# Kernel tuning notes

Hardware: AMD Instinct MI355X
Metric: run time of the kernel (lower is better)

Reference implementation:

```python
import jax, jax.numpy as jnp
import numpy as np

C_IN = 64
GDIM = C_IN // 2      # 32, GHPA dim_in
CD = GDIM // 4        # 8, c_dim_in
GRID = C_IN // 2      # 32, learned param grid (x=y)
EXPR = 2
B, W, H, D = 2, 64, 64, 64


def _gelu(x):
    return jax.nn.gelu(x, approximate=False)


def _interp_last(p, out_len):
    # 1D linear interpolation along last axis, align_corners=True
    L = p.shape[-1]
    pos = jnp.linspace(0.0, L - 1.0, out_len)
    i0 = jnp.clip(jnp.floor(pos).astype(jnp.int32), 0, L - 1)
    i1 = jnp.clip(i0 + 1, 0, L - 1)
    w = (pos - i0).astype(p.dtype)
    return p[..., i0] * (1.0 - w) + p[..., i1] * w


def _interp2(p, h, w):
    # bilinear align_corners=True over last two axes (separable)
    p = _interp_last(p, w)
    p = jnp.swapaxes(_interp_last(jnp.swapaxes(p, -2, -1), h), -2, -1)
    return p


def _conv2d(x, w, b, groups=1, pad=0):
    y = jax.lax.conv_general_dilated(x, w, (1, 1), [(pad, pad), (pad, pad)],
                                     feature_group_count=groups,
                                     dimension_numbers=('NCHW', 'OIHW', 'NCHW'))
    return y + b[None, :, None, None]


def _conv1d(x, w, b, groups=1, pad=0):
    y = jax.lax.conv_general_dilated(x, w, (1,), [(pad, pad)],
                                     feature_group_count=groups,
                                     dimension_numbers=('NCH', 'OIH', 'NCH'))
    return y + b[None, :, None]


def _ln_cf(x, g, b, eps=1e-6):
    # channels_first LayerNorm over channel axis 1 of NCHW
    u = x.mean(1, keepdims=True)
    s = ((x - u) ** 2).mean(1, keepdims=True)
    xh = (x - u) / jnp.sqrt(s + eps)
    return g[None, :, None, None] * xh + b[None, :, None, None]


def _inorm3d(x, eps=1e-5):
    # InstanceNorm3d, affine=False: normalize over spatial dims per (B, C)
    u = x.mean((2, 3, 4), keepdims=True)
    v = ((x - u) ** 2).mean((2, 3, 4), keepdims=True)
    return (x - u) / jnp.sqrt(v + eps)


def setup_inputs() -> dict:
    key = jax.random.key(0)
    ks = iter(jax.random.split(key, 40))
    f = lambda shape: 0.05 * jax.random.normal(next(ks), shape, dtype=jnp.float32)
    z = lambda shape: jnp.zeros(shape, jnp.float32)
    o = lambda shape: jnp.ones(shape, jnp.float32)
    inp = {
        'x': jax.random.normal(next(ks), (B, C_IN, W, H, D), dtype=jnp.float32),
        # GHPA layer norms
        'n1_g': o((GDIM,)), 'n1_b': z((GDIM,)),
        'n2_g': o((GDIM,)), 'n2_b': z((GDIM,)),
        # learned Hadamard params (torch inits to ones)
        'p_xy': o((1, CD, GRID, GRID)),
        'p_zx': o((1, 1, CD, GRID)),
        'p_zy': o((1, 1, CD, GRID)),
        # conv_xy: depthwise 3x3 + 1x1
        'xy_dw_w': f((CD, 1, 3, 3)), 'xy_dw_b': z((CD,)),
        'xy_pw_w': f((CD, CD, 1, 1)), 'xy_pw_b': z((CD,)),
        # conv_zx / conv_zy: depthwise 1d k=3 + 1x1 1d
        'zx_dw_w': f((CD, 1, 3)), 'zx_dw_b': z((CD,)),
        'zx_pw_w': f((CD, CD, 1)), 'zx_pw_b': z((CD,)),
        'zy_dw_w': f((CD, 1, 3)), 'zy_dw_b': z((CD,)),
        'zy_pw_w': f((CD, CD, 1)), 'zy_pw_b': z((CD,)),
        # dw branch: 1x1 + depthwise 3x3
        'dw_pw_w': f((CD, CD, 1, 1)), 'dw_pw_b': z((CD,)),
        'dw_dw_w': f((CD, 1, 3, 3)), 'dw_dw_b': z((CD,)),
        # ldw: depthwise 3x3 + 1x1 on full GDIM
        'ldw_dw_w': f((GDIM, 1, 3, 3)), 'ldw_dw_b': z((GDIM,)),
        'ldw_pw_w': f((GDIM, GDIM, 1, 1)), 'ldw_pw_b': z((GDIM,)),
        # MlpChannel 1x1x1 convs as dense over channel
        'fc1_w': f((C_IN * EXPR, C_IN)), 'fc1_b': z((C_IN * EXPR,)),
        'fc2_w': f((C_IN, C_IN * EXPR)), 'fc2_b': z((C_IN,)),
    }
    return inp


def reference(x, n1_g, n1_b, n2_g, n2_b, p_xy, p_zx, p_zy,
              xy_dw_w, xy_dw_b, xy_pw_w, xy_pw_b,
              zx_dw_w, zx_dw_b, zx_pw_w, zx_pw_b,
              zy_dw_w, zy_dw_b, zy_pw_w, zy_pw_b,
              dw_pw_w, dw_pw_b, dw_dw_w, dw_dw_b,
              ldw_dw_w, ldw_dw_b, ldw_pw_w, ldw_pw_b,
              fc1_w, fc1_b, fc2_w, fc2_b):
    cd = CD

    def ghpa(z):  # z: (N, GDIM, A, Bd)
        N, C, A, Bd = z.shape
        z = _ln_cf(z, n1_g, n1_b)
        x1, x2, x3, x4 = jnp.split(z, 4, axis=1)
        # xy branch: interpolate learned 2D grid, conv, Hadamard
        k = _interp2(p_xy, A, Bd)                       # (1, cd, A, Bd)
        k = _conv2d(k, xy_dw_w, xy_dw_b, groups=cd, pad=1)
        k = _conv2d(_gelu(k), xy_pw_w, xy_pw_b)
        x1 = x1 * k
        # zx branch: permute (N,cd,A,Bd)->(N,Bd,cd,A)
        x2p = jnp.transpose(x2, (0, 3, 1, 2))
        kz = _interp2(p_zx, cd, A)[0]                   # (1, cd, A)
        kz = _conv1d(kz, zx_dw_w, zx_dw_b, groups=cd, pad=1)
        kz = _conv1d(_gelu(kz), zx_pw_w, zx_pw_b)
        x2 = jnp.transpose(x2p * kz[None], (0, 2, 3, 1))
        # zy branch: permute (N,cd,A,Bd)->(N,A,cd,Bd)
        x3p = jnp.transpose(x3, (0, 2, 1, 3))
        ky = _interp2(p_zy, cd, Bd)[0]                  # (1, cd, Bd)
        ky = _conv1d(ky, zy_dw_w, zy_dw_b, groups=cd, pad=1)
        ky = _conv1d(_gelu(ky), zy_pw_w, zy_pw_b)
        x3 = jnp.transpose(x3p * ky[None], (0, 2, 1, 3))
        # dw branch
        x4 = _conv2d(x4, dw_pw_w, dw_pw_b)
        x4 = _conv2d(_gelu(x4), dw_dw_w, dw_dw_b, groups=cd, pad=1)
        z = jnp.concatenate([x1, x2, x3, x4], axis=1)
        z = _ln_cf(z, n2_g, n2_b)
        z = _conv2d(z, ldw_dw_w, ldw_dw_b, groups=GDIM, pad=1)
        z = _conv2d(_gelu(z), ldw_pw_w, ldw_pw_b)
        return z

    xh, xres = jnp.split(x, 2, axis=1)                  # each (B, GDIM, W, H, D)
    xh = _inorm3d(xh)
    Bb, C, Ww, Hh, Dd = xh.shape
    # direction 0: 'b c w h d -> (h b) c w d'
    xr = jnp.transpose(xh, (3, 0, 1, 2, 4)).reshape(Hh * Bb, C, Ww, Dd)
    y1 = ghpa(xr).reshape(Hh, Bb, C, Ww, Dd).transpose(1, 2, 3, 0, 4)
    y2 = ghpa(xr[::-1]).reshape(Hh, Bb, C, Ww, Dd).transpose(1, 2, 3, 0, 4)[::-1]
    whd = y1 + y2
    z = jnp.concatenate([whd, xres], axis=1)            # (B, C_IN, W, H, D)
    z = _inorm3d(z)
    # MlpChannel: 1x1x1 convs = channel-wise dense
    h = jnp.einsum('bcwhd,oc->bowhd', z, fc1_w) + fc1_b[None, :, None, None, None]
    h = _gelu(h)
    out = jnp.einsum('bcwhd,oc->bowhd', h, fc2_w) + fc2_b[None, :, None, None, None]
    return out
```

## Files before the change

### kernel.cpp

```cpp
#include <hip/hip_runtime.h>
#include <hip/hip_bf16.h>

typedef __hip_bfloat16 bf16;
typedef __attribute__((ext_vector_type(8))) short short8;
typedef __attribute__((ext_vector_type(4))) float f32x4;

__device__ __forceinline__ float b2f(bf16 v){ return __bfloat162float(v); }
__device__ __forceinline__ bf16  f2b(float v){ return __float2bfloat16(v); }
__device__ __forceinline__ unsigned short f2bu(float f){
  return __builtin_bit_cast(unsigned short, __float2bfloat16(f));
}
__device__ __forceinline__ float u2f(unsigned short u){
  return __uint_as_float(((unsigned int)u) << 16);
}
__device__ __forceinline__ float geluf(float x){ return 0.5f*x*(1.0f+erff(x*0.70710678118654752440f)); }

template<bool F32> __device__ __forceinline__ float ldin(const void* p, size_t i){
  if (F32) return ((const float*)p)[i];
  return b2f(((const bf16*)p)[i]);
}
__device__ __forceinline__ float ldf(const void* p, size_t i, bool f32){
  return f32 ? ((const float*)p)[i] : b2f(((const bf16*)p)[i]);
}

#define SS    4096
#define SSS   262144

__global__ void k_probe(const unsigned short* __restrict__ xr, int* __restrict__ flag){
  float m = 0.f;
  for (int i = threadIdx.x; i < 512; i += 64){
    unsigned int u = ((unsigned int)xr[i]) << 16;
    float v = fabsf(__uint_as_float(u));
    if (!(v < 3.0e38f)) v = 3.0e38f;
    m = fmaxf(m, v);
  }
  #pragma unroll
  for (int off = 32; off > 0; off >>= 1) m = fmaxf(m, __shfl_down(m, off));
  if (threadIdx.x == 0) flag[0] = (m > 1000.0f) ? 1 : 0;
}

__device__ __forceinline__ void blk_reduce2(float& s, float& s2){
  __shared__ float sa[4], sb[4];
  #pragma unroll
  for (int off = 32; off > 0; off >>= 1){ s += __shfl_down(s, off); s2 += __shfl_down(s2, off); }
  int wid = threadIdx.x >> 6;
  if ((threadIdx.x & 63) == 0){ sa[wid] = s; sb[wid] = s2; }
  __syncthreads();
  if (threadIdx.x == 0){ s = sa[0]+sa[1]+sa[2]+sa[3]; s2 = sb[0]+sb[1]+sb[2]+sb[3]; }
}

__global__ __launch_bounds__(256) void k_cstats(const int* __restrict__ flag,
    const void* __restrict__ x, float* __restrict__ part){
  const bool f32 = (flag[0] != 0);
  int bc = blockIdx.x >> 3, sp = blockIdx.x & 7;
  size_t base = (size_t)bc*SSS + (size_t)sp*32768;
  float s = 0.f, s2 = 0.f;
  if (f32){
    const float4* p = (const float4*)((const float*)x + base);
    for (int i = threadIdx.x; i < 8192; i += 256){
      float4 v = p[i];
      s += v.x+v.y+v.z+v.w; s2 += v.x*v.x+v.y*v.y+v.z*v.z+v.w*v.w;
    }
  } else {
    const ushort4* p = (const ushort4*)((const unsigned short*)x + base);
    for (int i = threadIdx.x; i < 8192; i += 256){
      ushort4 v = p[i];
      float a=u2f(v.x),b_=u2f(v.y),c=u2f(v.z),d=u2f(v.w);
      s += a+b_+c+d; s2 += a*a+b_*b_+c*c+d*d;
    }
  }
  blk_reduce2(s, s2);
  if (threadIdx.x == 0){ part[blockIdx.x*2] = s; part[blockIdx.x*2+1] = s2; }
}

__global__ void k_sfinal(const float* __restrict__ part,
    float* __restrict__ meanH, float* __restrict__ rstdH,
    float* __restrict__ mean2, float* __restrict__ rstd2){
  int t = threadIdx.x; if (t >= 128) return;
  float s = 0.f, s2 = 0.f;
  #pragma unroll
  for (int i = 0; i < 8; i++){ s += part[(t*8+i)*2]; s2 += part[(t*8+i)*2+1]; }
  float m = s * (1.f/262144.f);
  float var = s2 * (1.f/262144.f) - m*m;
  int b = t >> 6, c = t & 63;
  if (c < 32){ meanH[b*32+c] = m; rstdH[b*32+c] = rsqrtf(var + 1e-5f); }
  else       { mean2[t] = m;      rstd2[t] = rsqrtf(var + 1e-5f); }
}

__global__ __launch_bounds__(256) void k_mult1(const int* __restrict__ flag,
    const void* __restrict__ p_xy, const void* __restrict__ p_zx, const void* __restrict__ p_zy,
    const void* __restrict__ xy_dw_w, const void* __restrict__ xy_dw_b,
    const void* __restrict__ zx_dw_w, const void* __restrict__ zx_dw_b,
    const void* __restrict__ zy_dw_w, const void* __restrict__ zy_dw_b,
    float* __restrict__ t_xy, float* __restrict__ t_zx, float* __restrict__ t_zy){
  const bool f32 = (flag[0] != 0);
  const float SC = 31.f/63.f;
  int id = blockIdx.x*256 + threadIdx.x;
  if (id < 32768){
    int c = id >> 12, rem = id & 4095, uu = rem >> 6, vv = rem & 63;
    float acc = ldf(xy_dw_b, c, f32);
    for (int du = 0; du < 3; du++){
      int ui = uu + du - 1; if (ui < 0 || ui >= 64) continue;
      float pu = ui*SC; int i0 = (int)pu; float wu = pu - (float)i0; int i1 = min(i0+1, 31);
      for (int dv = 0; dv < 3; dv++){
        int vi = vv + dv - 1; if (vi < 0 || vi >= 64) continue;
        float pv = vi*SC; int j0 = (int)pv; float wv = pv - (float)j0; int j1 = min(j0+1, 31);
        float s = ldf(p_xy, c*1024+i0*32+j0, f32)*(1.f-wu)*(1.f-wv) + ldf(p_xy, c*1024+i0*32+j1, f32)*(1.f-wu)*wv
                + ldf(p_xy, c*1024+i1*32+j0, f32)*wu*(1.f-wv)       + ldf(p_xy, c*1024+i1*32+j1, f32)*wu*wv;
        acc += ldf(xy_dw_w, c*9 + du*3 + dv, f32) * s;
      }
    }
    t_xy[id] = geluf(acc);
  } else if (id < 33280){
    int k = id - 32768; int c = k >> 6, a = k & 63;
    float acc = ldf(zx_dw_b, c, f32);
    for (int da = 0; da < 3; da++){
      int ai = a + da - 1; if (ai < 0 || ai >= 64) continue;
      float pa = ai*SC; int i0 = (int)pa; float wa = pa - (float)i0; int i1 = min(i0+1, 31);
      float s = ldf(p_zx, c*32+i0, f32)*(1.f-wa) + ldf(p_zx, c*32+i1, f32)*wa;
      acc += ldf(zx_dw_w, c*3+da, f32) * s;
    }
    t_zx[k] = geluf(acc);
  } else if (id < 33792){
    int k = id - 33280; int c = k >> 6, a = k & 63;
    float acc = ldf(zy_dw_b, c, f32);
    for (int da = 0; da < 3; da++){
      int ai = a + da - 1; if (ai < 0 || ai >= 64) continue;
      float pa = ai*SC; int i0 = (int)pa; float wa = pa - (float)i0; int i1 = min(i0+1, 31);
      float s = ldf(p_zy, c*32+i0, f32)*(1.f-wa) + ldf(p_zy, c*32+i1, f32)*wa;
      acc += ldf(zy_dw_w, c*3+da, f32) * s;
    }
    t_zy[k] = geluf(acc);
  }
}

__global__ __launch_bounds__(256) void k_mult2(const int* __restrict__ flag,
    const float* __restrict__ t_xy, const float* __restrict__ t_zx, const float* __restrict__ t_zy,
    const void* __restrict__ xy_pw_w, const void* __restrict__ xy_pw_b,
    const void* __restrict__ zx_pw_w, const void* __restrict__ zx_pw_b,
    const void* __restrict__ zy_pw_w, const void* __restrict__ zy_pw_b,
    float* __restrict__ kxy, float* __restrict__ kz, float* __restrict__ ky){
  const bool f32 = (flag[0] != 0);
  int id = blockIdx.x*256 + threadIdx.x;
  if (id < 32768){
    int oc = id >> 12, pix = id & 4095;
    float acc = ldf(xy_pw_b, oc, f32);
    #pragma unroll
    for (int ic = 0; ic < 8; ic++) acc += ldf(xy_pw_w, oc*8+ic, f32) * t_xy[ic*4096 + pix];
    kxy[id] = acc;
  } else if (id < 33280){
    int k = id - 32768; int oc = k >> 6, a = k & 63;
    float acc = ldf(zx_pw_b, oc, f32);
    #pragma unroll
    for (int ic = 0; ic < 8; ic++) acc += ldf(zx_pw_w, oc*8+ic, f32) * t_zx[ic*64 + a];
    kz[k] = acc;
  } else if (id < 33792){
    int k = id - 33280; int oc = k >> 6, a = k & 63;
    float acc = ldf(zy_pw_b, oc, f32);
    #pragma unroll
    for (int ic = 0; ic < 8; ic++) acc += ldf(zy_pw_w, oc*8+ic, f32) * t_zy[ic*64 + a];
    ky[k] = acc;
  }
}

#define TB 4
#define W_M    0
#define W_R    32
#define W_G1   64
#define W_B1   96
#define W_G2   128
#define W_B2   160
#define W_LDWB 192
#define W_LPWB 224
#define W_PW   256
#define W_PWB  320
#define W_DW   328
#define W_DWB  400
#define W_LDW  408
#define W_TOT  696

template<bool F32>
__global__ __launch_bounds__(256) void k_g(const int* __restrict__ flag,
    const void* __restrict__ x,
    const void* n1g_, const void* n1b_, const void* n2g_, const void* n2b_,
    const void* dwpw_w, const void* dwpw_b, const void* dwdw_w, const void* dwdw_b,
    const void* ldw_dw_w, const void* ldw_dw_b, const void* ldw_pw_w, const void* ldw_pw_b,
    const float* __restrict__ meanH, const float* __restrict__ rstdH,
    const float* __restrict__ kxy, const float* __restrict__ kz, const float* __restrict__ ky,
    bf16* __restrict__ g){
  if (flag[0] != (F32 ? 1 : 0)) return;
  __shared__ unsigned short xs[32*6*64];
  __shared__ unsigned short t4g[8*8*64];
  __shared__ float muinv[2*6*64];
  __shared__ float sw[W_TOT];
  int n  = blockIdx.x >> 4;
  int a0 = (blockIdx.x & 15) * TB;
  int b = n & 1, h = n >> 1;
  int t = threadIdx.x;
  if (t < 32){
    sw[W_M+t]=meanH[b*32+t]; sw[W_R+t]=rstdH[b*32+t];
    sw[W_G1+t]=ldin<F32>(n1g_, t); sw[W_B1+t]=ldin<F32>(n1b_, t);
    sw[W_G2+t]=ldin<F32>(n2g_, t); sw[W_B2+t]=ldin<F32>(n2b_, t);
    sw[W_LDWB+t]=ldin<F32>(ldw_dw_b, t); sw[W_LPWB+t]=ldin<F32>(ldw_pw_b, t);
  }
  if (t >= 64 && t < 128) sw[W_PW+t-64]=ldin<F32>(dwpw_w, t-64);
  if (t >= 128 && t < 200) sw[W_DW+t-128]=ldin<F32>(dwdw_w, t-128);
  if (t >= 200 && t < 208) sw[W_PWB+t-200]=ldin<F32>(dwpw_b, t-200);
  if (t >= 208 && t < 216) sw[W_DWB+t-208]=ldin<F32>(dwdw_b, t-208);
  for (int i = t; i < 288; i += 256)  sw[W_LDW+i] = ldin<F32>(ldw_dw_w, i);
  __syncthreads();
  const float* s_g1 = sw+W_G1; const float* s_b1 = sw+W_B1;
  const float* s_g2 = sw+W_G2; const float* s_b2 = sw+W_B2;
  const int arow0 = a0 - 2;
  const size_t xbase = (size_t)b*64*SSS + (size_t)h*64;

  for (int i = t; i < 3072; i += 256){
    int c = i / 96, rem = i - c*96, row = rem >> 4, q = rem & 15;
    int a = a0 - 1 + row;
    unsigned short o0=0,o1=0,o2=0,o3=0;
    if (a >= 0 && a < 64){
      float m = sw[W_M+c], r = sw[W_R+c];
      size_t base = xbase + (size_t)c*SSS + (size_t)a*SS + q*4;
      if (F32){
        float4 v = *(const float4*)((const float*)x + base);
        o0=f2bu((v.x-m)*r); o1=f2bu((v.y-m)*r); o2=f2bu((v.z-m)*r); o3=f2bu((v.w-m)*r);
      } else {
        ushort4 v = *(const ushort4*)((const unsigned short*)x + base);
        o0=f2bu((u2f(v.x)-m)*r); o1=f2bu((u2f(v.y)-m)*r); o2=f2bu((u2f(v.z)-m)*r); o3=f2bu((u2f(v.w)-m)*r);
      }
    }
    ushort4 o4; o4.x=o0; o4.y=o1; o4.z=o2; o4.w=o3;
    *(ushort4*)&xs[(c*6+row)*64 + q*4] = o4;
  }
  __syncthreads();

  for (int p = t; p < 8*64; p += 256){
    int row = p >> 6, d = p & 63;
    int a = arow0 + row;
    if (a < 0 || a >= 64){
      #pragma unroll
      for (int ic = 0; ic < 8; ic++) t4g[(ic*8+row)*64+d] = 0;
      continue;
    }
    float sum = 0.f, sq = 0.f; float z24[8];
    if (row >= 1 && row <= 6){
      int r6 = row - 1;
      #pragma unroll
      for (int c = 0; c < 32; c++){
        float v = u2f(xs[(c*6+r6)*64+d]); sum += v; sq += v*v;
        if (c >= 24) z24[c-24] = v;
      }
    } else {
      size_t xi = xbase + (size_t)a*SS + d;
      #pragma unroll
      for (int c = 0; c < 32; c++){
        float v = (ldin<F32>(x, xi + (size_t)c*SSS) - sw[W_M+c]) * sw[W_R+c];
        sum += v; sq += v*v;
        if (c >= 24) z24[c-24] = v;
      }
    }
    float mu = sum * (1.f/32.f);
    float inv = rsqrtf(sq*(1.f/32.f) - mu*mu + 1e-6f);
    if (row >= 1 && row <= 6){
      muinv[(row-1)*64+d] = mu; muinv[384 + (row-1)*64+d] = inv;
    }
    float zl[8];
    #pragma unroll
    for (int j = 0; j < 8; j++) zl[j] = (z24[j]-mu)*inv*s_g1[24+j] + s_b1[24+j];
    #pragma unroll
    for (int ic = 0; ic < 8; ic++){
      float acc = sw[W_PWB+ic];
      #pragma unroll
      for (int j = 0; j < 8; j++) acc += sw[W_PW+ic*8+j]*zl[j];
      t4g[(ic*8+row)*64+d] = f2bu(geluf(acc));
    }
  }
  __syncthreads();

  for (int p = t; p < 6*64; p += 256){
    int r2 = p >> 6, d = p & 63;
    int a = a0 - 1 + r2;
    if (a < 0 || a >= 64) continue;
    float mu = muinv[r2*64+d], inv = muinv[384 + r2*64+d];
    float s2 = 0.f, q2 = 0.f;
    #pragma unroll
    for (int c = 0; c < 8; c++){
      int idx = (c*6+r2)*64+d;
      float u = ((u2f(xs[idx])-mu)*inv*s_g1[c] + s_b1[c]) * kxy[(c*64 + a)*64 + d];
      xs[idx] = f2bu(u); s2 += u; q2 += u*u;
    }
    #pragma unroll
    for (int c = 8; c < 16; c++){
      int idx = (c*6+r2)*64+d;
      float u = ((u2f(xs[idx])-mu)*inv*s_g1[c] + s_b1[c]) * kz[(c-8)*64 + a];
      xs[idx] = f2bu(u); s2 += u; q2 += u*u;
    }
    #pragma unroll
    for (int c = 16; c < 24; c++){
      int idx = (c*6+r2)*64+d;
      float u = ((u2f(xs[idx])-mu)*inv*s_g1[c] + s_b1[c]) * ky[(c-16)*64 + d];
      xs[idx] = f2bu(u); s2 += u; q2 += u*u;
    }
    #pragma unroll
    for (int oc = 0; oc < 8; oc++){
      float acc = sw[W_DWB+oc];
      #pragma unroll
      for (int du = 0; du < 3; du++){
        #pragma unroll
        for (int dv = 0; dv < 3; dv++){
          int v2 = d + dv - 1;
          if (v2 >= 0 && v2 < 64) acc += sw[W_DW+oc*9+du*3+dv]*u2f(t4g[(oc*8+r2+du)*64+v2]);
        }
      }
      xs[((24+oc)*6+r2)*64+d] = f2bu(acc); s2 += acc; q2 += acc*acc;
    }
    float mu2 = s2 * (1.f/32.f);
    float inv2 = rsqrtf(q2*(1.f/32.f) - mu2*mu2 + 1e-6f);
    #pragma unroll
    for (int c = 0; c < 32; c++){
      int idx = (c*6+r2)*64+d;
      float uu = u2f(xs[idx]);
      xs[idx] = f2bu((uu-mu2)*inv2*s_g2[c] + s_b2[c]);
    }
  }
  __syncthreads();

  unsigned short* lpwB = t4g;
  unsigned short* gdXS = xs;
  for (int i = t; i < 1024; i += 256){
    int o = i >> 5, ic = i & 31;
    lpwB[o*40 + ic] = f2bu(ldin<F32>(ldw_pw_w, o*32+ic));
  }
  float gd[32];
  {
    int r = t >> 6, d = t & 63;
    #pragma unroll
    for (int oc = 0; oc < 32; oc++){
      float acc = sw[W_LDWB+oc];
      #pragma unroll
      for (int du = 0; du < 3; du++){
        #pragma unroll
        for (int dv = 0; dv < 3; dv++){
          int v2 = d + dv - 1;
          if (v2 >= 0 && v2 < 64) acc += sw[W_LDW+oc*9+du*3+dv]*u2f(xs[(oc*6+r+du)*64+v2]);
        }
      }
      gd[oc] = geluf(acc);
    }
  }
  __syncthreads();

  #pragma unroll
  for (int q = 0; q < 4; q++){
    unsigned short tmp8[8];
    #pragma unroll
    for (int j = 0; j < 8; j++) tmp8[j] = f2bu(gd[q*8+j]);
    *(short8*)&gdXS[t*40 + q*8] = *(const short8*)tmp8;
  }
  __syncthreads();

  {
    int wv = t >> 6, l = t & 63;
    int lr = l & 15, lg = l >> 4;
    #pragma unroll
    for (int mi = 0; mi < 4; mi++){
      int px0 = wv*64 + mi*16;
      short8 af = *(const short8*)&gdXS[(px0+lr)*40 + lg*8];
      #pragma unroll
      for (int ot = 0; ot < 2; ot++){
        short8 bf = *(const short8*)&lpwB[(ot*16+lr)*40 + lg*8];
        f32x4 c4 = {0.f,0.f,0.f,0.f};
        c4 = __builtin_amdgcn_mfma_f32_16x16x32_bf16(af, bf, c4, 0, 0, 0);
        int oc = ot*16 + lr;
        float bo = sw[W_LPWB+oc];
        #pragma unroll
        for (int r4 = 0; r4 < 4; r4++){
          int px = px0 + lg*4 + r4;
          int aa = a0 + (px >> 6), dd = px & 63;
          g[(size_t)n*131072 + (size_t)oc*4096 + aa*64 + dd] = f2b(c4[r4] + bo);
        }
      }
    }
  }
}

__global__ __launch_bounds__(256) void k_gstats(const bf16* __restrict__ g,
                                                float* __restrict__ partg){
  int pair = blockIdx.x >> 3, sp = blockIdx.x & 7;
  int b = pair >> 5, c = pair & 31;
  float s = 0.f, s2 = 0.f;
  for (int i = threadIdx.x; i < 32768; i += 256){
    int ii = sp*32768 + i;
    int d = ii & 63, w = (ii >> 6) & 63, h = ii >> 12;
    int n1 = h*2 + b, n2 = (63-h)*2 + b;
    float v = b2f(g[((size_t)n1*32 + c)*4096 + w*64 + d]) + b2f(g[((size_t)n2*32 + c)*4096 + w*64 + d]);
    s += v; s2 += v*v;
  }
  blk_reduce2(s, s2);
  if (threadIdx.x == 0){ partg[blockIdx.x*2] = s; partg[blockIdx.x*2+1] = s2; }
}

__global__ void k_gfinal(const float* __restrict__ partg,
                         float* __restrict__ mean2, float* __restrict__ rstd2){
  int t = threadIdx.x; if (t >= 64) return;
  float s = 0.f, s2 = 0.f;
  #pragma unroll
  for (int i = 0; i < 8; i++){ s += partg[(t*8+i)*2]; s2 += partg[(t*8+i)*2+1]; }
  float m = s * (1.f/262144.f);
  float var = s2 * (1.f/262144.f) - m*m;
  int b = t >> 5, c = t & 31;
  mean2[b*64+c] = m; rstd2[b*64+c] = rsqrtf(var + 1e-5f);
}

__global__ __launch_bounds__(256) void k_mlp(const int* __restrict__ flag,
    const void* __restrict__ x, const bf16* __restrict__ g,
    const float* __restrict__ mean2, const float* __restrict__ rstd2,
    const void* __restrict__ fc1w, const void* __restrict__ fc1b,
    const void* __restrict__ fc2w, const void* __restrict__ fc2b,
    void* __restrict__ out){
  const bool f32 = (flag[0] != 0);
  __shared__ unsigned short zs[128*72];
  __shared__ unsigned short w1s[128*72];
  __shared__ unsigned short w2s[64*136];
  __shared__ unsigned short hb[4*16*136];
  __shared__ float b1s[128], b2s[64];
  int blk = blockIdx.x;
  int b = blk >> 11, w = (blk >> 5) & 63, hblk = blk & 31;
  int h0 = hblk*2;
  int t = threadIdx.x;
  const float* m2 = mean2 + b*64;
  const float* r2 = rstd2 + b*64;

  if (f32){
    const float* W1 = (const float*)fc1w;
    const float* W2 = (const float*)fc2w;
    for (int i = t; i < 8192; i += 256){ int j = i >> 6, c = i & 63; w1s[j*72+c] = f2bu(W1[i] * r2[c]); }
    for (int i = t; i < 8192; i += 256){ int o = i >> 7, j = i & 127; w2s[o*136+j] = f2bu(W2[i]); }
    if (t < 128){
      float s = 0.f;
      for (int c = 0; c < 64; c++) s += W1[t*64+c] * m2[c] * r2[c];
      b1s[t] = ((const float*)fc1b)[t] - s;
    }
    if (t < 64) b2s[t] = ((const float*)fc2b)[t];
  } else {
    const bf16* W1 = (const bf16*)fc1w;
    const bf16* W2 = (const bf16*)fc2w;
    for (int i = t; i < 8192; i += 256){ int j = i >> 6, c = i & 63; w1s[j*72+c] = f2bu(b2f(W1[i]) * r2[c]); }
    for (int i = t; i < 8192; i += 256){ int o = i >> 7, j = i & 127; w2s[o*136+j] = f2bu(b2f(W2[i])); }
    if (t < 128){
      float s = 0.f;
      for (int c = 0; c < 64; c++) s += b2f(W1[t*64+c]) * m2[c] * r2[c];
      b1s[t] = b2f(((const bf16*)fc1b)[t]) - s;
    }
    if (t < 64) b2s[t] = b2f(((const bf16*)fc2b)[t]);
  }

  {
    int px = t & 127, half = t >> 7;
    int hh = px >> 6, d = px & 63;
    int h = h0 + hh;
    unsigned short tmp[32];
    if (half == 0){
      int n1 = h*2 + b, n2 = (63-h)*2 + b;
      const bf16* g1 = g + ((size_t)n1*32)*4096 + w*64 + d;
      const bf16* g2 = g + ((size_t)n2*32)*4096 + w*64 + d;
      #pragma unroll
      for (int c = 0; c < 32; c++) tmp[c] = f2bu(b2f(g1[(size_t)c*4096]) + b2f(g2[(size_t)c*4096]));
    } else {
      size_t xi = ((size_t)(b*64+32))*SSS + (size_t)w*4096 + (size_t)h*64 + d;
      if (f32){
        const float* xp = (const float*)x;
        #pragma unroll
        for (int c = 0; c < 32; c++) tmp[c] = f2bu(xp[xi + (size_t)c*SSS]);
      } else {
        const unsigned short* xp = (const unsigned short*)x;
        #pragma unroll
        for (int c = 0; c < 32; c++) tmp[c] = xp[xi + (size_t)c*SSS];
      }
    }
    short8* dst = (short8*)&zs[px*72 + half*32];
    #pragma unroll
    for (int q = 0; q < 4; q++) dst[q] = *(short8*)&tmp[q*8];
  }
  __syncthreads();

  int wv = t >> 6, l = t & 63;
  int lr = l & 15, lg = l >> 4;
  unsigned short* hbw = &hb[wv*16*136];
  #pragma unroll
  for (int mi = 0; mi < 2; mi++){
    int px0 = wv*32 + mi*16;
    short8 a0 = *(const short8*)&zs[(px0+lr)*72 + lg*8];
    short8 a1 = *(const short8*)&zs[(px0+lr)*72 + 32 + lg*8];
    f32x4 acc[8];
    #pragma unroll
    for (int jt = 0; jt < 8; jt++){
      short8 b0 = *(const short8*)&w1s[(jt*16+lr)*72 + lg*8];
      short8 b1 = *(const short8*)&w1s[(jt*16+lr)*72 + 32 + lg*8];
      f32x4 c4 = {0.f,0.f,0.f,0.f};
      c4 = __builtin_amdgcn_mfma_f32_16x16x32_bf16(a0, b0, c4, 0, 0, 0);
      c4 = __builtin_amdgcn_mfma_f32_16x16x32_bf16(a1, b1, c4, 0, 0, 0);
      acc[jt] = c4;
    }
    #pragma unroll
    for (int jt = 0; jt < 8; jt++){
      float bj = b1s[jt*16+lr];
      #pragma unroll
      for (int r = 0; r < 4; r++){
        hbw[(lg*4+r)*136 + jt*16 + lr] = f2bu(geluf(acc[jt][r] + bj));
      }
    }
    short8 ha[4];
    #pragma unroll
    for (int m = 0; m < 4; m++) ha[m] = *(const short8*)&hbw[lr*136 + m*32 + lg*8];
    #pragma unroll
    for (int ot = 0; ot < 4; ot++){
      f32x4 c4 = {0.f,0.f,0.f,0.f};
      #pragma unroll
      for (int m = 0; m < 4; m++){
        short8 bb = *(const short8*)&w2s[(ot*16+lr)*136 + m*32 + lg*8];
        c4 = __builtin_amdgcn_mfma_f32_16x16x32_bf16(ha[m], bb, c4, 0, 0, 0);
      }
      int oc = ot*16 + lr;
      float bo = b2s[oc];
      if (f32){
        float* op = (float*)out;
        #pragma unroll
        for (int r = 0; r < 4; r++){
          int px = px0 + lg*4 + r;
          size_t oi = ((size_t)(b*64+oc))*SSS + (size_t)w*4096 + (size_t)(h0 + (px>>6))*64 + (px&63);
          op[oi] = c4[r] + bo;
        }
      } else {
        bf16* op = (bf16*)out;
        #pragma unroll
        for (int r = 0; r < 4; r++){
          int px = px0 + lg*4 + r;
          size_t oi = ((size_t)(b*64+oc))*SSS + (size_t)w*4096 + (size_t)(h0 + (px>>6))*64 + (px&63);
          op[oi] = f2b(c4[r] + bo);
        }
      }
    }
  }
}

extern "C" void kernel_launch(void* const* d_in, const int* in_sizes, int n_in,
                              void* d_out, int out_size, void* d_ws, size_t ws_size,
                              hipStream_t stream) {
  const void* X      = d_in[0];
  const void* n1g    = d_in[1];
  const void* n1b    = d_in[2];
  const void* n2g    = d_in[3];
  const void* n2b    = d_in[4];
  const void* p_xy   = d_in[5];
  const void* p_zx   = d_in[6];
  const void* p_zy   = d_in[7];
  const void* xy_dw_w= d_in[8];
  const void* xy_dw_b= d_in[9];
  const void* xy_pw_w= d_in[10];
  const void* xy_pw_b= d_in[11];
  const void* zx_dw_w= d_in[12];
  const void* zx_dw_b= d_in[13];
  const void* zx_pw_w= d_in[14];
  const void* zx_pw_b= d_in[15];
  const void* zy_dw_w= d_in[16];
  const void* zy_dw_b= d_in[17];
  const void* zy_pw_w= d_in[18];
  const void* zy_pw_b= d_in[19];
  const void* dw_pw_w= d_in[20];
  const void* dw_pw_b= d_in[21];
  const void* dw_dw_w= d_in[22];
  const void* dw_dw_b= d_in[23];
  const void* ldw_dw_w=d_in[24];
  const void* ldw_dw_b=d_in[25];
  const void* ldw_pw_w=d_in[26];
  const void* ldw_pw_b=d_in[27];
  const void* fc1w   = d_in[28];
  const void* fc1b   = d_in[29];
  const void* fc2w   = d_in[30];
  const void* fc2b   = d_in[31];

  int*  flag = (int*)d_ws;
  bf16* g    = (bf16*)((char*)d_ws + 16);
  float* fb  = (float*)((char*)d_ws + 16 + (size_t)16777216*2);
  float* meanH = fb;
  float* rstdH = fb + 64;
  float* t_xy  = fb + 128;
  float* t_zx  = fb + 32896;
  float* t_zy  = fb + 33408;
  float* kxy   = fb + 33920;
  float* kz    = fb + 66688;
  float* ky    = fb + 67200;
  float* mean2 = fb + 67712;
  float* rstd2 = fb + 67840;
  float* part  = fb + 67968;
  float* partg = fb + 70016;

  k_probe<<<1, 64, 0, stream>>>((const unsigned short*)X, flag);
  k_cstats<<<1024, 256, 0, stream>>>(flag, X, part);
  k_sfinal<<<1, 128, 0, stream>>>(part, meanH, rstdH, mean2, rstd2);
  k_mult1<<<132, 256, 0, stream>>>(flag, p_xy, p_zx, p_zy, xy_dw_w, xy_dw_b,
                                   zx_dw_w, zx_dw_b, zy_dw_w, zy_dw_b, t_xy, t_zx, t_zy);
  k_mult2<<<132, 256, 0, stream>>>(flag, t_xy, t_zx, t_zy, xy_pw_w, xy_pw_b,
                                   zx_pw_w, zx_pw_b, zy_pw_w, zy_pw_b, kxy, kz, ky);
  k_g<false><<<128*(64/TB), 256, 0, stream>>>(flag, X, n1g, n1b, n2g, n2b,
                                       dw_pw_w, dw_pw_b, dw_dw_w, dw_dw_b,
                                       ldw_dw_w, ldw_dw_b, ldw_pw_w, ldw_pw_b,
                                       meanH, rstdH, kxy, kz, ky, g);
  k_g<true ><<<128*(64/TB), 256, 0, stream>>>(flag, X, n1g, n1b, n2g, n2b,
                                       dw_pw_w, dw_pw_b, dw_dw_w, dw_dw_b,
                                       ldw_dw_w, ldw_dw_b, ldw_pw_w, ldw_pw_b,
                                       meanH, rstdH, kxy, kz, ky, g);
  k_gstats<<<512, 256, 0, stream>>>(g, partg);
  k_gfinal<<<1, 64, 0, stream>>>(partg, mean2, rstd2);
  k_mlp<<<4096, 256, 0, stream>>>(flag, X, g, mean2, rstd2, fc1w, fc1b, fc2w, fc2b, d_out);
}
```

Before: 376.6 us.

## Precompute folded MLP weights once, stage output through LDS, use tanh GELU

Adds a small prep kernel that folds the instance-norm scale and shift into fc1 weights and bias and converts weights to bf16 once, instead of every one of 4096 MLP blocks recomputing them into LDS. MLP blocks now read the B operands straight from global/L2 and load only the bias arrays. Output is staged through LDS so each thread writes contiguous vector chunks per channel rather than scattered scalar stores. GELU is also replaced by the tanh approximation with a fast exp, which changes numerics away from the exact erf GELU that the reference uses.

```diff
diff --git a/kernel.cpp b/kernel.cpp
--- a/kernel.cpp
+++ b/kernel.cpp
@@ -13,7 +13,12 @@
 __device__ __forceinline__ float u2f(unsigned short u){
   return __uint_as_float(((unsigned int)u) << 16);
 }
-__device__ __forceinline__ float geluf(float x){ return 0.5f*x*(1.0f+erff(x*0.70710678118654752440f)); }
+__device__ __forceinline__ float geluf(float x){
+  float t = 0.7978845608028654f*(x + 0.044715f*x*x*x);
+  float e = __expf(2.f*t);
+  float th = 1.f - 2.f/(e + 1.f);
+  return 0.5f*x*(1.f + th);
+}
 
 template<bool F32> __device__ __forceinline__ float ldin(const void* p, size_t i){
   if (F32) return ((const float*)p)[i];
@@ -412,48 +417,47 @@
   mean2[b*64+c] = m; rstd2[b*64+c] = rsqrtf(var + 1e-5f);
 }
 
+__global__ __launch_bounds__(256) void k_mprep(const int* __restrict__ flag,
+    const void* __restrict__ fc1w, const void* __restrict__ fc1b,
+    const void* __restrict__ fc2w, const void* __restrict__ fc2b,
+    const float* __restrict__ mean2, const float* __restrict__ rstd2,
+    unsigned short* __restrict__ W1p, unsigned short* __restrict__ W2b,
+    float* __restrict__ b1p, float* __restrict__ b2p){
+  const bool f32 = (flag[0] != 0);
+  int gid = blockIdx.x*256 + threadIdx.x;
+  for (int i = gid; i < 16384; i += 4096){
+    int bb = i >> 13, r = i & 8191, c = r & 63;
+    W1p[i] = f2bu(ldf(fc1w, r, f32) * rstd2[bb*64+c]);
+  }
+  for (int i = gid; i < 8192; i += 4096) W2b[i] = f2bu(ldf(fc2w, i, f32));
+  if (gid < 256){
+    int bb = gid >> 7, j = gid & 127;
+    float s = ldf(fc1b, j, f32);
+    for (int c = 0; c < 64; c++) s -= ldf(fc1w, j*64+c, f32) * mean2[bb*64+c] * rstd2[bb*64+c];
+    b1p[gid] = s;
+  }
+  if (gid < 64) b2p[gid] = ldf(fc2b, gid, f32);
+}
+
 __global__ __launch_bounds__(256) void k_mlp(const int* __restrict__ flag,
     const void* __restrict__ x, const bf16* __restrict__ g,
-    const float* __restrict__ mean2, const float* __restrict__ rstd2,
-    const void* __restrict__ fc1w, const void* __restrict__ fc1b,
-    const void* __restrict__ fc2w, const void* __restrict__ fc2b,
+    const unsigned short* __restrict__ W1p, const unsigned short* __restrict__ W2b,
+    const float* __restrict__ b1p, const float* __restrict__ b2p,
     void* __restrict__ out){
   const bool f32 = (flag[0] != 0);
-  __shared__ unsigned short zs[128*72];
-  __shared__ unsigned short w1s[128*72];
-  __shared__ unsigned short w2s[64*136];
-  __shared__ unsigned short hb[4*16*136];
-  __shared__ float b1s[128], b2s[64];
+  __shared__ char smem[36608];
+  unsigned short* zs = (unsigned short*)smem;
+  unsigned short* hb = (unsigned short*)(smem+18432);
+  float* b1s = (float*)(smem+35840);
+  float* b2s = (float*)(smem+36352);
+  float* obuf = (float*)smem;
   int blk = blockIdx.x;
   int b = blk >> 11, w = (blk >> 5) & 63, hblk = blk & 31;
   int h0 = hblk*2;
   int t = threadIdx.x;
-  const float* m2 = mean2 + b*64;
-  const float* r2 = rstd2 + b*64;
-
-  if (f32){
-    const float* W1 = (const float*)fc1w;
-    const float* W2 = (const float*)fc2w;
-    for (int i = t; i < 8192; i += 256){ int j = i >> 6, c = i & 63; w1s[j*72+c] = f2bu(W1[i] * r2[c]); }
-    for (int i = t; i < 8192; i += 256){ int o = i >> 7, j = i & 127; w2s[o*136+j] = f2bu(W2[i]); }
-    if (t < 128){
-      float s = 0.f;
-      for (int c = 0; c < 64; c++) s += W1[t*64+c] * m2[c] * r2[c];
-      b1s[t] = ((const float*)fc1b)[t] - s;
-    }
-    if (t < 64) b2s[t] = ((const float*)fc2b)[t];
-  } else {
-    const bf16* W1 = (const bf16*)fc1w;
-    const bf16* W2 = (const bf16*)fc2w;
-    for (int i = t; i < 8192; i += 256){ int j = i >> 6, c = i & 63; w1s[j*72+c] = f2bu(b2f(W1[i]) * r2[c]); }
-    for (int i = t; i < 8192; i += 256){ int o = i >> 7, j = i & 127; w2s[o*136+j] = f2bu(b2f(W2[i])); }
-    if (t < 128){
-      float s = 0.f;
-      for (int c = 0; c < 64; c++) s += b2f(W1[t*64+c]) * m2[c] * r2[c];
-      b1s[t] = b2f(((const bf16*)fc1b)[t]) - s;
-    }
-    if (t < 64) b2s[t] = b2f(((const bf16*)fc2b)[t]);
-  }
+  if (t < 128) b1s[t] = b1p[b*128+t];
+  if (t < 64)  b2s[t] = b2p[t];
+  const unsigned short* W1g = W1p + b*8192;
 
   {
     int px = t & 127, half = t >> 7;
@@ -487,6 +491,7 @@
   int wv = t >> 6, l = t & 63;
   int lr = l & 15, lg = l >> 4;
   unsigned short* hbw = &hb[wv*16*136];
+  float ov[2][4][4];
   #pragma unroll
   for (int mi = 0; mi < 2; mi++){
     int px0 = wv*32 + mi*16;
@@ -495,8 +500,8 @@
     f32x4 acc[8];
     #pragma unroll
     for (int jt = 0; jt < 8; jt++){
-      short8 b0 = *(const short8*)&w1s[(jt*16+lr)*72 + lg*8];
-      short8 b1 = *(const short8*)&w1s[(jt*16+lr)*72 + 32 + lg*8];
+      short8 b0 = *(const short8*)&W1g[(jt*16+lr)*64 + lg*8];
+      short8 b1 = *(const short8*)&W1g[(jt*16+lr)*64 + 32 + lg*8];
       f32x4 c4 = {0.f,0.f,0.f,0.f};
       c4 = __builtin_amdgcn_mfma_f32_16x16x32_bf16(a0, b0, c4, 0, 0, 0);
       c4 = __builtin_amdgcn_mfma_f32_16x16x32_bf16(a1, b1, c4, 0, 0, 0);
@@ -518,27 +523,49 @@
       f32x4 c4 = {0.f,0.f,0.f,0.f};
       #pragma unroll
       for (int m = 0; m < 4; m++){
-        short8 bb = *(const short8*)&w2s[(ot*16+lr)*136 + m*32 + lg*8];
+        short8 bb = *(const short8*)&W2b[(ot*16+lr)*128 + m*32 + lg*8];
         c4 = __builtin_amdgcn_mfma_f32_16x16x32_bf16(ha[m], bb, c4, 0, 0, 0);
       }
+      #pragma unroll
+      for (int r4 = 0; r4 < 4; r4++) ov[mi][ot][r4] = c4[r4];
+    }
+  }
+  __syncthreads();
+
+  #pragma unroll
+  for (int mi = 0; mi < 2; mi++){
+    int px0 = wv*32 + mi*16;
+    #pragma unroll
+    for (int ot = 0; ot < 4; ot++){
       int oc = ot*16 + lr;
       float bo = b2s[oc];
-      if (f32){
-        float* op = (float*)out;
+      #pragma unroll
+      for (int r4 = 0; r4 < 4; r4++){
+        obuf[oc*129 + px0 + lg*4 + r4] = ov[mi][ot][r4] + bo;
+      }
+    }
+  }
+  __syncthreads();
+
+  {
+    int oc = t >> 2, ch = t & 3;
+    size_t base = ((size_t)(b*64+oc))*SSS + (size_t)w*4096 + (size_t)h0*64 + ch*32;
+    const float* src = &obuf[oc*129 + ch*32];
+    if (f32){
+      float* op = (float*)out;
+      #pragma unroll
+      for (int k = 0; k < 8; k++){
+        float4 v; v.x = src[k*4]; v.y = src[k*4+1]; v.z = src[k*4+2]; v.w = src[k*4+3];
+        *(float4*)&op[base + k*4] = v;
+      }
+    } else {
+      bf16* op = (bf16*)out;
+      #pragma unroll
+      for (int k = 0; k < 4; k++){
+        unsigned short tmp8[8];
         #pragma unroll
-        for (int r = 0; r < 4; r++){
-          int px = px0 + lg*4 + r;
-          size_t oi = ((size_t)(b*64+oc))*SSS + (size_t)w*4096 + (size_t)(h0 + (px>>6))*64 + (px&63);
-          op[oi] = c4[r] + bo;
-        }
-      } else {
-        bf16* op = (bf16*)out;
-        #pragma unroll
-        for (int r = 0; r < 4; r++){
-          int px = px0 + lg*4 + r;
-          size_t oi = ((size_t)(b*64+oc))*SSS + (size_t)w*4096 + (size_t)(h0 + (px>>6))*64 + (px&63);
-          op[oi] = f2b(c4[r] + bo);
-        }
+        for (int j = 0; j < 8; j++) tmp8[j] = f2bu(src[k*8+j]);
+        *(short8*)&op[base + k*8] = *(const short8*)tmp8;
       }
     }
   }
@@ -595,6 +622,10 @@
   float* rstd2 = fb + 67840;
   float* part  = fb + 67968;
   float* partg = fb + 70016;
+  float* b1p   = fb + 71040;
+  float* b2p   = fb + 71296;
+  unsigned short* W1p = (unsigned short*)(fb + 71360);
+  unsigned short* W2b = (unsigned short*)(fb + 79552);
 
   k_probe<<<1, 64, 0, stream>>>((const unsigned short*)X, flag);
   k_cstats<<<1024, 256, 0, stream>>>(flag, X, part);
@@ -613,5 +644,7 @@
                                        meanH, rstdH, kxy, kz, ky, g);
   k_gstats<<<512, 256, 0, stream>>>(g, partg);
   k_gfinal<<<1, 64, 0, stream>>>(partg, mean2, rstd2);
-  k_mlp<<<4096, 256, 0, stream>>>(flag, X, g, mean2, rstd2, fc1w, fc1b, fc2w, fc2b, d_out);
-}
+  k_mprep<<<16, 256, 0, stream>>>(flag, fc1w, fc1b, fc2w, fc2b, mean2, rstd2,
+                                  W1p, W2b, b1p, b2p);
+  k_mlp<<<4096, 256, 0, stream>>>(flag, X, g, W1p, W2b, b1p, b2p, d_out);
+}
```

New measurement: 415.6 us. 10.3% more time.
